# Kernel tuning notes

Hardware: AMD Instinct MI355X
Metric: run time of the kernel (lower is better)

## Reference

```python
import jax, jax.numpy as jnp
import numpy as np

N_NODES = 100000
N_EDGES = 1600000
HID = 128


def setup_inputs() -> dict:
    key = jax.random.key(0)
    ks = jax.random.split(key, 16)

    def w(k, fan_in, fan_out, scale=None):
        s = scale if scale is not None else 1.0 / np.sqrt(fan_in)
        return (jax.random.normal(k, (fan_in, fan_out), jnp.float32) * s)

    inp = {
        "h": jax.random.normal(ks[0], (N_NODES, HID), jnp.float32),
        "edge_index": jax.random.randint(ks[1], (2, N_EDGES), 0, N_NODES, jnp.int64),
        "x": jax.random.normal(ks[2], (N_NODES, 3), jnp.float32),
        "v": jax.random.normal(ks[3], (N_NODES, 3), jnp.float32),
        # edge_mlp: Linear(257,128) -> ReLU -> Linear(128,128) -> ReLU
        "we1": w(ks[4], 2 * HID + 1, HID), "be1": jnp.zeros((HID,), jnp.float32),
        "we2": w(ks[5], HID, HID), "be2": jnp.zeros((HID,), jnp.float32),
        # node_mlp: Linear(384,128) -> ReLU -> Linear(128,128)
        "wn1": w(ks[6], 3 * HID, HID), "bn1": jnp.zeros((HID,), jnp.float32),
        "wn2": w(ks[7], HID, HID), "bn2": jnp.zeros((HID,), jnp.float32),
        # coord_mlp_vel: Linear(128,128) -> ReLU -> Linear(128,1)
        "wv1": w(ks[8], HID, HID), "bv1": jnp.zeros((HID,), jnp.float32),
        "wv2": w(ks[9], HID, 1), "bv2": jnp.zeros((1,), jnp.float32),
        # coord_mlp: Linear(128,128) -> ReLU -> Linear(128,1, bias=False, xavier gain 0.001)
        "wc1": w(ks[10], HID, HID), "bc1": jnp.zeros((HID,), jnp.float32),
        "wc2": w(ks[11], HID, 1, scale=0.001),
    }
    return inp


def reference(h, edge_index, x, v, we1, be1, we2, be2, wn1, bn1, wn2, bn2,
              wv1, bv1, wv2, bv2, wc1, bc1, wc2):
    n = h.shape[0]
    row, col = edge_index[0], edge_index[1]

    # coord2radial
    coord_diff = x[row] - x[col]                                  # [M, 3]
    radial = jnp.sum(coord_diff * coord_diff, axis=1, keepdims=True)  # [M, 1]

    # edge_model (no attention, no edge_attr)
    e_in = jnp.concatenate([h[row], h[col], radial], axis=1)      # [M, 257]
    edge_feat = jax.nn.relu(jax.nn.relu(e_in @ we1 + be1) @ we2 + be2)  # [M, 128]

    # coord_model: per-edge scalar gate, clamp, segment-mean over row
    gate = jax.nn.relu(edge_feat @ wc1 + bc1) @ wc2               # [M, 1]
    trans = jnp.clip(coord_diff * gate, -100.0, 100.0)            # [M, 3]
    num = jax.ops.segment_sum(trans, row, num_segments=n)         # [N, 3]
    cnt = jax.ops.segment_sum(jnp.ones_like(trans), row, num_segments=n)
    f = (num / jnp.maximum(cnt, 1.0)) * 1.0                       # coords_weight = 1.0

    # update: v' = gate(h) * v + f ; x' = x + v'
    vel_gate = jax.nn.relu(h @ wv1 + bv1) @ wv2 + bv2             # [N, 1]
    v_new = vel_gate * v + f
    x_new = x + v_new

    # node_model with others=h: cat[h, h, segment_sum(edge_feat)]
    agg = jax.ops.segment_sum(edge_feat, row, num_segments=n)     # [N, 128]
    n_in = jnp.concatenate([h, h, agg], axis=1)                   # [N, 384]
    h_new = h + (jax.nn.relu(n_in @ wn1 + bn1) @ wn2 + bn2)       # recurrent residual

    return h_new, x_new, v_new
```

## Files before the change

kernel.cpp:

```cpp
#include <hip/hip_runtime.h>
#include <hip/hip_bf16.h>
#include <stdint.h>

typedef __bf16 bf16_t;
typedef __bf16 bf16x8 __attribute__((ext_vector_type(8)));
typedef float f32x4 __attribute__((ext_vector_type(4)));

#define HID 128

__device__ __forceinline__ bf16_t* swz(bf16_t* base, int row, int rowBytes, int byteInRow) {
    return (bf16_t*)((char*)base + row * rowBytes + (byteInRow ^ ((row & 7) << 4)));
}
__device__ __forceinline__ const bf16_t* swzc(const bf16_t* base, int row, int rowBytes, int byteInRow) {
    return (const bf16_t*)((const char*)base + row * rowBytes + (byteInRow ^ ((row & 7) << 4)));
}

__device__ __forceinline__ bf16x8 pack8(float4 a, float4 b) {
    bf16x8 r;
    r[0] = (bf16_t)a.x; r[1] = (bf16_t)a.y; r[2] = (bf16_t)a.z; r[3] = (bf16_t)a.w;
    r[4] = (bf16_t)b.x; r[5] = (bf16_t)b.y; r[6] = (bf16_t)b.z; r[7] = (bf16_t)b.w;
    return r;
}

__device__ __forceinline__ bool is_i64(const int* ei) {
    return ((ei[1] | ei[3] | ei[5] | ei[7]) == 0);
}
__device__ __forceinline__ int eidx(const int* __restrict__ ei, int i, bool i64) {
    return i64 ? ei[2 * i] : ei[i];
}

__global__ void prep_kernel(const float* __restrict__ we1, const float* __restrict__ we2,
                            const float* __restrict__ wc1, const float* __restrict__ wn1,
                            const float* __restrict__ wn2, const float* __restrict__ wv1,
                            bf16_t* w1t, float* w1last, bf16_t* w2t, bf16_t* wc1t,
                            bf16_t* wn1t, bf16_t* wn2t, bf16_t* wv1t) {
    int idx = blockIdx.x * 256 + threadIdx.x;
    if (idx < 32768) { int j = idx >> 8, k = idx & 255; w1t[idx] = (bf16_t)we1[k * 128 + j]; return; }
    idx -= 32768;
    if (idx < 128) { w1last[idx] = we1[256 * 128 + idx]; return; }
    idx -= 128;
    if (idx < 16384) { int j = idx >> 7, k = idx & 127; w2t[idx] = (bf16_t)we2[k * 128 + j]; return; }
    idx -= 16384;
    if (idx < 16384) { int j = idx >> 7, k = idx & 127; wc1t[idx] = (bf16_t)wc1[k * 128 + j]; return; }
    idx -= 16384;
    if (idx < 32768) {
        int j = idx >> 8, k = idx & 255;
        float val = (k < 128) ? (wn1[k * 128 + j] + wn1[(k + 128) * 128 + j])
                              : wn1[(k + 128) * 128 + j];
        wn1t[idx] = (bf16_t)val; return;
    }
    idx -= 32768;
    if (idx < 16384) { int j = idx >> 7, k = idx & 127; wn2t[idx] = (bf16_t)wn2[k * 128 + j]; return; }
    idx -= 16384;
    if (idx < 16384) { int j = idx >> 7, k = idx & 127; wv1t[idx] = (bf16_t)wv1[k * 128 + j]; return; }
}

__global__ void hist_kernel(const int* __restrict__ ei, int* __restrict__ hist, int M) {
    const bool i64 = is_i64(ei);
    int e = blockIdx.x * 256 + threadIdx.x;
    if (e < M) atomicAdd(&hist[eidx(ei, e, i64)], 1);
}

#define NCHUNK 128
__global__ void scanA_kernel(const int* __restrict__ hist, int* __restrict__ chunk_sums,
                             int N, int CHUNK) {
    __shared__ int red[256];
    int b = blockIdx.x, tid = threadIdx.x;
    int lo = b * CHUNK, hi = min(N, lo + CHUNK);
    int s = 0;
    for (int i = lo + tid; i < hi; i += 256) s += hist[i];
    red[tid] = s; __syncthreads();
    for (int ofs = 128; ofs > 0; ofs >>= 1) {
        if (tid < ofs) red[tid] += red[tid + ofs];
        __syncthreads();
    }
    if (tid == 0) chunk_sums[b] = red[0];
}

__global__ void scanB_kernel(const int* __restrict__ chunk_sums, int* __restrict__ chunk_base,
                             int* __restrict__ off, int N, int M) {
    __shared__ int s[NCHUNK];
    int tid = threadIdx.x;
    if (tid < NCHUNK) s[tid] = chunk_sums[tid];
    __syncthreads();
    if (tid == 0) {
        int run = 0;
        for (int i = 0; i < NCHUNK; i++) { int v = s[i]; s[i] = run; run += v; }
        off[N] = M;
    }
    __syncthreads();
    if (tid < NCHUNK) chunk_base[tid] = s[tid];
}

__global__ void scanC_kernel(const int* __restrict__ hist, const int* __restrict__ chunk_base,
                             int* __restrict__ off, int* __restrict__ cursor, int N, int CHUNK) {
    __shared__ int sd[256];
    int b = blockIdx.x, tid = threadIdx.x;
    int carry = chunk_base[b];
    for (int base = 0; base < CHUNK; base += 256) {
        int li = base + tid;
        int i = b * CHUNK + li;
        int v = (li < CHUNK && i < N) ? hist[i] : 0;
        sd[tid] = v; __syncthreads();
        for (int ofs = 1; ofs < 256; ofs <<= 1) {
            int t = (tid >= ofs) ? sd[tid - ofs] : 0;
            __syncthreads();
            sd[tid] += t;
            __syncthreads();
        }
        int excl = sd[tid] - v;
        if (li < CHUNK && i < N) { off[i] = carry + excl; cursor[i] = carry + excl; }
        carry += sd[255];
        __syncthreads();
    }
}

__global__ void scatter_kernel(const int* __restrict__ ei, int* __restrict__ cursor,
                               int* __restrict__ sorted_eid, int* __restrict__ sorted_row, int M) {
    const bool i64 = is_i64(ei);
    int e = blockIdx.x * 256 + threadIdx.x;
    if (e < M) {
        int r = eidx(ei, e, i64);
        int p = atomicAdd(&cursor[r], 1);
        sorted_eid[p] = e;
        sorted_row[p] = r;
    }
}

__global__ __launch_bounds__(512, 2) void edge_kernel(
    const float* __restrict__ h, const int* __restrict__ ei, const float* __restrict__ x,
    const float* __restrict__ be1, const float* __restrict__ be2,
    const float* __restrict__ bc1, const float* __restrict__ wc2,
    const bf16_t* __restrict__ w1t, const float* __restrict__ w1last,
    const bf16_t* __restrict__ w2t, const bf16_t* __restrict__ wc1t,
    const int* __restrict__ sorted_eid, const int* __restrict__ sorted_row,
    float* __restrict__ agg, float* __restrict__ num,
    int M, int N) {
    __shared__ bf16_t lw1[128 * 256];
    __shared__ bf16_t lw2[128 * 128];
    __shared__ bf16_t lbuf[8][2][16 * 128];

    const int tid = threadIdx.x;
    for (int c = tid; c < 4096; c += 512) {
        int row = c >> 5, cin = c & 31;
        *(float4*)swz(lw1, row, 512, cin * 16) = ((const float4*)w1t)[c];
    }
    for (int c = tid; c < 2048; c += 512) {
        int row = c >> 4, cin = c & 15;
        *(float4*)swz(lw2, row, 256, cin * 16) = ((const float4*)w2t)[c];
    }
    __syncthreads();

    const bool i64 = is_i64(ei);
    const int wave = tid >> 6, lane = tid & 63;
    const int l15 = lane & 15, l4 = lane >> 4;
    bf16_t* b0 = lbuf[wave][0];
    bf16_t* b1 = lbuf[wave][1];
    const int wid = blockIdx.x * 8 + wave;
    const int nw = gridDim.x * 8;
    const int ntiles = M >> 4;
    const int K = (ntiles + nw - 1) / nw;
    const int tb = wid * K;
    const int te = min(ntiles, tb + K);

    const int c0 = lane, c1 = lane + 64;
    int carryRow = -1;
    float cs0 = 0.f, cs1 = 0.f;

    for (int t = tb; t < te; t++) {
        const int e0 = t << 4;
        const int s = lane >> 2, p = lane & 3;
        const int er = sorted_row[e0 + s];
        const int eid = sorted_eid[e0 + s];
        const int ec = eidx(ei, M + eid, i64);
        const float* hr = h + (size_t)er * HID + p * 32;
        const float* hc = h + (size_t)ec * HID + p * 32;
#pragma unroll
        for (int c2 = 0; c2 < 4; c2++) {
            float4 a = *(const float4*)(hr + c2 * 8);
            float4 b = *(const float4*)(hr + c2 * 8 + 4);
            *(bf16x8*)swz(b0, s, 256, (p * 4 + c2) * 16) = pack8(a, b);
        }
#pragma unroll
        for (int c2 = 0; c2 < 4; c2++) {
            float4 a = *(const float4*)(hc + c2 * 8);
            float4 b = *(const float4*)(hc + c2 * 8 + 4);
            *(bf16x8*)swz(b1, s, 256, (p * 4 + c2) * 16) = pack8(a, b);
        }
        float d0 = x[er * 3 + 0] - x[ec * 3 + 0];
        float d1 = x[er * 3 + 1] - x[ec * 3 + 1];
        float d2 = x[er * 3 + 2] - x[ec * 3 + 2];
        float radial = d0 * d0 + d1 * d1 + d2 * d2;
        __builtin_amdgcn_wave_barrier();

        float rad4[4];
#pragma unroll
        for (int r = 0; r < 4; r++) rad4[r] = __shfl(radial, (l4 * 4 + r) * 4, 64);

        f32x4 acc[8];
#pragma unroll
        for (int n = 0; n < 8; n++) {
            int j = n * 16 + l15;
            float bb = be1[j], wl = w1last[j];
#pragma unroll
            for (int r = 0; r < 4; r++) acc[n][r] = bb + rad4[r] * wl;
        }
#pragma unroll
        for (int kk = 0; kk < 8; kk++) {
            const bf16_t* ab = (kk < 4) ? b0 : b1;
            bf16x8 af = *(const bf16x8*)swzc(ab, l15, 256, (kk & 3) * 64 + l4 * 16);
#pragma unroll
            for (int n = 0; n < 8; n++) {
                bf16x8 bf = *(const bf16x8*)swzc(lw1, n * 16 + l15, 512, kk * 64 + l4 * 16);
                acc[n] = __builtin_amdgcn_mfma_f32_16x16x32_bf16(af, bf, acc[n], 0, 0, 0);
            }
        }
#pragma unroll
        for (int n = 0; n < 8; n++) {
#pragma unroll
            for (int r = 0; r < 4; r++) {
                int rw = l4 * 4 + r;
                *swz(b0, rw, 256, (n * 16 + l15) * 2) = (bf16_t)fmaxf(acc[n][r], 0.f);
            }
        }
        __builtin_amdgcn_wave_barrier();

        f32x4 acc2[8];
#pragma unroll
        for (int n = 0; n < 8; n++) {
            float bb = be2[n * 16 + l15];
#pragma unroll
            for (int r = 0; r < 4; r++) acc2[n][r] = bb;
        }
#pragma unroll
        for (int kk = 0; kk < 4; kk++) {
            bf16x8 af = *(const bf16x8*)swzc(b0, l15, 256, kk * 64 + l4 * 16);
#pragma unroll
            for (int n = 0; n < 8; n++) {
                bf16x8 bf = *(const bf16x8*)swzc(lw2, n * 16 + l15, 256, kk * 64 + l4 * 16);
                acc2[n] = __builtin_amdgcn_mfma_f32_16x16x32_bf16(af, bf, acc2[n], 0, 0, 0);
            }
        }
#pragma unroll
        for (int n = 0; n < 8; n++) {
#pragma unroll
            for (int r = 0; r < 4; r++) {
                float v_ = fmaxf(acc2[n][r], 0.f);
                int rw = l4 * 4 + r;
                *swz(b1, rw, 256, (n * 16 + l15) * 2) = (bf16_t)v_;
            }
        }
        __builtin_amdgcn_wave_barrier();

        f32x4 acc3[8];
#pragma unroll
        for (int n = 0; n < 8; n++) {
            float bb = bc1[n * 16 + l15];
#pragma unroll
            for (int r = 0; r < 4; r++) acc3[n][r] = bb;
        }
#pragma unroll
        for (int kk = 0; kk < 4; kk++) {
            bf16x8 af = *(const bf16x8*)swzc(b1, l15, 256, kk * 64 + l4 * 16);
#pragma unroll
            for (int n = 0; n < 8; n++) {
                bf16x8 bf = *(const bf16x8*)(wc1t + (n * 16 + l15) * 128 + kk * 32 + l4 * 8);
                acc3[n] = __builtin_amdgcn_mfma_f32_16x16x32_bf16(af, bf, acc3[n], 0, 0, 0);
            }
        }
        float pr[4] = {0.f, 0.f, 0.f, 0.f};
#pragma unroll
        for (int n = 0; n < 8; n++) {
            float w = wc2[n * 16 + l15];
#pragma unroll
            for (int r = 0; r < 4; r++) pr[r] += fmaxf(acc3[n][r], 0.f) * w;
        }
#pragma unroll
        for (int m = 1; m < 16; m <<= 1) {
#pragma unroll
            for (int r = 0; r < 4; r++) pr[r] += __shfl_xor(pr[r], m, 16);
        }

        {
            int s3 = s & 3;
            float g = (s3 == 0) ? pr[0] : ((s3 == 1) ? pr[1] : ((s3 == 2) ? pr[2] : pr[3]));
            if ((lane & 3) == 0) {
                float t0 = fminf(fmaxf(d0 * g, -100.f), 100.f);
                float t1 = fminf(fmaxf(d1 * g, -100.f), 100.f);
                float t2 = fminf(fmaxf(d2 * g, -100.f), 100.f);
                atomicAdd(num + (size_t)er * 3 + 0, t0);
                atomicAdd(num + (size_t)er * 3 + 1, t1);
                atomicAdd(num + (size_t)er * 3 + 2, t2);
            }
        }

        int er16[16];
#pragma unroll
        for (int rw = 0; rw < 16; rw++) er16[rw] = __shfl(er, rw * 4, 64);

#pragma unroll
        for (int rw = 0; rw < 16; rw++) {
            int r = er16[rw];
            if (r != carryRow) {
                if (carryRow >= 0) {
                    atomicAdd(agg + (size_t)carryRow * HID + c0, cs0);
                    atomicAdd(agg + (size_t)carryRow * HID + c1, cs1);
                }
                carryRow = r; cs0 = 0.f; cs1 = 0.f;
            }
            cs0 += (float)*swzc(b1, rw, 256, c0 * 2);
            cs1 += (float)*swzc(b1, rw, 256, c1 * 2);
        }
        __builtin_amdgcn_wave_barrier();
    }
    if (carryRow >= 0) {
        atomicAdd(agg + (size_t)carryRow * HID + c0, cs0);
        atomicAdd(agg + (size_t)carryRow * HID + c1, cs1);
    }
}

__global__ __launch_bounds__(1024, 4) void node_kernel(
    const float* __restrict__ h, const float* __restrict__ x, const float* __restrict__ v,
    const float* __restrict__ bn1, const float* __restrict__ bn2,
    const float* __restrict__ bv1, const float* __restrict__ bv2,
    const float* __restrict__ wv2,
    const bf16_t* __restrict__ wn1t, const bf16_t* __restrict__ wn2t,
    const bf16_t* __restrict__ wv1t,
    const float* __restrict__ num, const int* __restrict__ off,
    float* __restrict__ out_h, float* __restrict__ out_x, float* __restrict__ out_v,
    int N) {
    __shared__ bf16_t lw1[128 * 256];
    __shared__ bf16_t lw2[128 * 128];
    __shared__ bf16_t lbuf[16][16 * 128];

    const int tid = threadIdx.x;
    for (int c = tid; c < 4096; c += 1024) {
        int row = c >> 5, cin = c & 31;
        *(float4*)swz(lw1, row, 512, cin * 16) = ((const float4*)wn1t)[c];
    }
    for (int c = tid; c < 2048; c += 1024) {
        int row = c >> 4, cin = c & 15;
        *(float4*)swz(lw2, row, 256, cin * 16) = ((const float4*)wn2t)[c];
    }
    __syncthreads();

    const int wave = tid >> 6, lane = tid & 63;
    const int l15 = lane & 15, l4 = lane >> 4;
    bf16_t* b0 = lbuf[wave];
    const int wid = blockIdx.x * 16 + wave;
    const int stride = gridDim.x * 16;
    const int nt = N >> 4;

    for (int t = wid; t < nt; t += stride) {
        const int m0 = t << 4;
        const float* hb = h + (size_t)(m0 + l15) * HID;
        const float* ab = out_h + (size_t)(m0 + l15) * HID;

        f32x4 av[8];
#pragma unroll
        for (int n = 0; n < 8; n++) {
            float bb = bv1[n * 16 + l15];
#pragma unroll
            for (int r = 0; r < 4; r++) av[n][r] = bb;
        }
#pragma unroll
        for (int kk = 0; kk < 4; kk++) {
            const float* ap = hb + kk * 32 + l4 * 8;
            bf16x8 af = pack8(*(const float4*)ap, *(const float4*)(ap + 4));
#pragma unroll
            for (int n = 0; n < 8; n++) {
                bf16x8 bf = *(const bf16x8*)(wv1t + (n * 16 + l15) * 128 + kk * 32 + l4 * 8);
                av[n] = __builtin_amdgcn_mfma_f32_16x16x32_bf16(af, bf, av[n], 0, 0, 0);
            }
        }
        float pv[4] = {0.f, 0.f, 0.f, 0.f};
#pragma unroll
        for (int n = 0; n < 8; n++) {
            float w = wv2[n * 16 + l15];
#pragma unroll
            for (int r = 0; r < 4; r++) pv[r] += fmaxf(av[n][r], 0.f) * w;
        }
#pragma unroll
        for (int m = 1; m < 16; m <<= 1) {
#pragma unroll
            for (int r = 0; r < 4; r++) pv[r] += __shfl_xor(pv[r], m, 16);
        }
        float bv2v = bv2[0];
        if (l15 == 0) {
#pragma unroll
            for (int r = 0; r < 4; r++) {
                int m = m0 + l4 * 4 + r;
                float vg = pv[r] + bv2v;
                float c = (float)(off[m + 1] - off[m]);
                float inv = 1.0f / fmaxf(c, 1.0f);
#pragma unroll
                for (int i = 0; i < 3; i++) {
                    float f = num[(size_t)m * 3 + i] * inv;
                    float vn = vg * v[(size_t)m * 3 + i] + f;
                    out_v[(size_t)m * 3 + i] = vn;
                    out_x[(size_t)m * 3 + i] = x[(size_t)m * 3 + i] + vn;
                }
            }
        }

        f32x4 a1[8];
#pragma unroll
        for (int n = 0; n < 8; n++) {
            float bb = bn1[n * 16 + l15];
#pragma unroll
            for (int r = 0; r < 4; r++) a1[n][r] = bb;
        }
#pragma unroll
        for (int kk = 0; kk < 4; kk++) {
            const float* ap = hb + kk * 32 + l4 * 8;
            bf16x8 af = pack8(*(const float4*)ap, *(const float4*)(ap + 4));
#pragma unroll
            for (int n = 0; n < 8; n++) {
                bf16x8 bf = *(const bf16x8*)swzc(lw1, n * 16 + l15, 512, kk * 64 + l4 * 16);
                a1[n] = __builtin_amdgcn_mfma_f32_16x16x32_bf16(af, bf, a1[n], 0, 0, 0);
            }
        }
#pragma unroll
        for (int c2 = 0; c2 < 4; c2++) {
            const float* ap = ab + c2 * 32 + l4 * 8;
            float fa[8];
            *(float4*)fa = *(const float4*)ap;
            *(float4*)(fa + 4) = *(const float4*)(ap + 4);
            bf16x8 hi8, lo8;
#pragma unroll
            for (int i = 0; i < 8; i++) {
                bf16_t hi = (bf16_t)fa[i];
                hi8[i] = hi;
                lo8[i] = (bf16_t)(fa[i] - (float)hi);
            }
#pragma unroll
            for (int n = 0; n < 8; n++) {
                bf16x8 bfh = *(const bf16x8*)swzc(lw1, n * 16 + l15, 512, (4 + c2) * 64 + l4 * 16);
                a1[n] = __builtin_amdgcn_mfma_f32_16x16x32_bf16(hi8, bfh, a1[n], 0, 0, 0);
            }
#pragma unroll
            for (int n = 0; n < 8; n++) {
                bf16x8 bfl = *(const bf16x8*)swzc(lw1, n * 16 + l15, 512, (4 + c2) * 64 + l4 * 16);
                a1[n] = __builtin_amdgcn_mfma_f32_16x16x32_bf16(lo8, bfl, a1[n], 0, 0, 0);
            }
        }
#pragma unroll
        for (int n = 0; n < 8; n++) {
#pragma unroll
            for (int r = 0; r < 4; r++) {
                int rw = l4 * 4 + r;
                *swz(b0, rw, 256, (n * 16 + l15) * 2) = (bf16_t)fmaxf(a1[n][r], 0.f);
            }
        }
        __builtin_amdgcn_wave_barrier();

        f32x4 a2[8];
#pragma unroll
        for (int n = 0; n < 8; n++) {
            float bb = bn2[n * 16 + l15];
#pragma unroll
            for (int r = 0; r < 4; r++) a2[n][r] = bb;
        }
#pragma unroll
        for (int kk = 0; kk < 4; kk++) {
            bf16x8 af = *(const bf16x8*)swzc(b0, l15, 256, kk * 64 + l4 * 16);
#pragma unroll
            for (int n = 0; n < 8; n++) {
                bf16x8 bf = *(const bf16x8*)swzc(lw2, n * 16 + l15, 256, kk * 64 + l4 * 16);
                a2[n] = __builtin_amdgcn_mfma_f32_16x16x32_bf16(af, bf, a2[n], 0, 0, 0);
            }
        }
#pragma unroll
        for (int n = 0; n < 8; n++) {
            int j = n * 16 + l15;
#pragma unroll
            for (int r = 0; r < 4; r++) {
                int m = m0 + l4 * 4 + r;
                out_h[(size_t)m * HID + j] = h[(size_t)m * HID + j] + a2[n][r];
            }
        }
        __builtin_amdgcn_wave_barrier();
    }
}

extern "C" void kernel_launch(void* const* d_in, const int* in_sizes, int n_in,
                              void* d_out, int out_size, void* d_ws, size_t ws_size,
                              hipStream_t stream) {
    const float* h   = (const float*)d_in[0];
    const int*   ei  = (const int*)d_in[1];
    const float* x   = (const float*)d_in[2];
    const float* v   = (const float*)d_in[3];
    const float* we1 = (const float*)d_in[4];
    const float* be1 = (const float*)d_in[5];
    const float* we2 = (const float*)d_in[6];
    const float* be2 = (const float*)d_in[7];
    const float* wn1 = (const float*)d_in[8];
    const float* bn1 = (const float*)d_in[9];
    const float* wn2 = (const float*)d_in[10];
    const float* bn2 = (const float*)d_in[11];
    const float* wv1 = (const float*)d_in[12];
    const float* bv1 = (const float*)d_in[13];
    const float* wv2 = (const float*)d_in[14];
    const float* bv2 = (const float*)d_in[15];
    const float* wc1 = (const float*)d_in[16];
    const float* bc1 = (const float*)d_in[17];
    const float* wc2 = (const float*)d_in[18];

    const int N = in_sizes[0] / HID;
    const int M = in_sizes[1] / 2;

    float* out_h = (float*)d_out;
    float* out_x = out_h + (size_t)N * HID;
    float* out_v = out_x + (size_t)N * 3;

    char* ws = (char*)d_ws;
    auto align256 = [](size_t v) { return (v + 255) & ~(size_t)255; };
    size_t o = 0;
    bf16_t* w1t    = (bf16_t*)(ws + o); o += 65536;
    float*  w1last = (float*)(ws + o);  o += 512;
    bf16_t* w2t    = (bf16_t*)(ws + o); o += 32768;
    bf16_t* wc1t   = (bf16_t*)(ws + o); o += 32768;
    bf16_t* wn1t   = (bf16_t*)(ws + o); o += 65536;
    bf16_t* wn2t   = (bf16_t*)(ws + o); o += 32768;
    bf16_t* wv1t   = (bf16_t*)(ws + o); o += 32768;
    float*  num    = (float*)(ws + o);        o = align256(o + (size_t)N * 12);
    int*    hist   = (int*)(ws + o);          o = align256(o + (size_t)N * 4);
    int*    off    = (int*)(ws + o);          o = align256(o + (size_t)(N + 1) * 4);
    int*    cursor = (int*)(ws + o);          o = align256(o + (size_t)N * 4);
    int*    chunk_sums = (int*)(ws + o);      o = align256(o + NCHUNK * 4);
    int*    chunk_base = (int*)(ws + o);      o = align256(o + NCHUNK * 4);
    int*    sorted_eid = (int*)(ws + o);      o = align256(o + (size_t)M * 4);
    int*    sorted_row = (int*)(ws + o);      o = align256(o + (size_t)M * 4);

    const int CHUNK = (N + NCHUNK - 1) / NCHUNK;

    hipMemsetAsync(out_h, 0, (size_t)N * HID * sizeof(float), stream);
    hipMemsetAsync(num, 0, (size_t)N * 12, stream);
    hipMemsetAsync(hist, 0, (size_t)N * 4, stream);

    prep_kernel<<<513, 256, 0, stream>>>(we1, we2, wc1, wn1, wn2, wv1,
                                         w1t, w1last, w2t, wc1t, wn1t, wn2t, wv1t);
    hist_kernel<<<(M + 255) / 256, 256, 0, stream>>>(ei, hist, M);
    scanA_kernel<<<NCHUNK, 256, 0, stream>>>(hist, chunk_sums, N, CHUNK);
    scanB_kernel<<<1, 256, 0, stream>>>(chunk_sums, chunk_base, off, N, M);
    scanC_kernel<<<NCHUNK, 256, 0, stream>>>(hist, chunk_base, off, cursor, N, CHUNK);
    scatter_kernel<<<(M + 255) / 256, 256, 0, stream>>>(ei, cursor, sorted_eid, sorted_row, M);

    edge_kernel<<<256, 512, 0, stream>>>(h, ei, x, be1, be2, bc1, wc2,
                                         w1t, w1last, w2t, wc1t,
                                         sorted_eid, sorted_row,
                                         out_h, num, M, N);
    node_kernel<<<256, 1024, 0, stream>>>(h, x, v, bn1, bn2, bv1, bv2, wv2,
                                          wn1t, wn2t, wv1t, num, off,
                                          out_h, out_x, out_v, N);
}
```

Measured before the change: 1.597 ms.

## Halve per-wave LDS staging and raise edge kernel to 12 waves per block

The edge kernel now keeps one 16x128 bf16 LDS buffer per wave instead of two. The h[row] operand for the first GEMM is loaded straight from global memory into MFMA A-fragments rather than staged through LDS. The LDS this frees lets each block run 12 waves (768 threads), aimed at more latency hiding for the gathers and atomics. In exchange, the row features are read per fragment from global memory (sorted rows are often repeated and cached), registers are tighter under launch_bounds(768,3), and extra wave barriers are added for buffer reuse.

```diff
diff --git a/kernel.cpp b/kernel.cpp
--- a/kernel.cpp
+++ b/kernel.cpp
@@ -127,7 +127,7 @@
     }
 }
 
-__global__ __launch_bounds__(512, 2) void edge_kernel(
+__global__ __launch_bounds__(768, 3) void edge_kernel(
     const float* __restrict__ h, const int* __restrict__ ei, const float* __restrict__ x,
     const float* __restrict__ be1, const float* __restrict__ be2,
     const float* __restrict__ bc1, const float* __restrict__ wc2,
@@ -138,14 +138,14 @@
     int M, int N) {
     __shared__ bf16_t lw1[128 * 256];
     __shared__ bf16_t lw2[128 * 128];
-    __shared__ bf16_t lbuf[8][2][16 * 128];
+    __shared__ bf16_t lbuf[12][16 * 128];
 
     const int tid = threadIdx.x;
-    for (int c = tid; c < 4096; c += 512) {
+    for (int c = tid; c < 4096; c += 768) {
         int row = c >> 5, cin = c & 31;
         *(float4*)swz(lw1, row, 512, cin * 16) = ((const float4*)w1t)[c];
     }
-    for (int c = tid; c < 2048; c += 512) {
+    for (int c = tid; c < 2048; c += 768) {
         int row = c >> 4, cin = c & 15;
         *(float4*)swz(lw2, row, 256, cin * 16) = ((const float4*)w2t)[c];
     }
@@ -154,10 +154,9 @@
     const bool i64 = is_i64(ei);
     const int wave = tid >> 6, lane = tid & 63;
     const int l15 = lane & 15, l4 = lane >> 4;
-    bf16_t* b0 = lbuf[wave][0];
-    bf16_t* b1 = lbuf[wave][1];
-    const int wid = blockIdx.x * 8 + wave;
-    const int nw = gridDim.x * 8;
+    bf16_t* b0 = lbuf[wave];
+    const int wid = blockIdx.x * 12 + wave;
+    const int nw = gridDim.x * 12;
     const int ntiles = M >> 4;
     const int K = (ntiles + nw - 1) / nw;
     const int tb = wid * K;
@@ -169,27 +168,21 @@
 
     for (int t = tb; t < te; t++) {
         const int e0 = t << 4;
+        const int erl = sorted_row[e0 + l15];
         const int s = lane >> 2, p = lane & 3;
-        const int er = sorted_row[e0 + s];
-        const int eid = sorted_eid[e0 + s];
-        const int ec = eidx(ei, M + eid, i64);
-        const float* hr = h + (size_t)er * HID + p * 32;
-        const float* hc = h + (size_t)ec * HID + p * 32;
+        const int ers = sorted_row[e0 + s];
+        const int ecs = eidx(ei, M + sorted_eid[e0 + s], i64);
+
+        const float* hcs = h + (size_t)ecs * HID + p * 32;
 #pragma unroll
         for (int c2 = 0; c2 < 4; c2++) {
-            float4 a = *(const float4*)(hr + c2 * 8);
-            float4 b = *(const float4*)(hr + c2 * 8 + 4);
+            float4 a = *(const float4*)(hcs + c2 * 8);
+            float4 b = *(const float4*)(hcs + c2 * 8 + 4);
             *(bf16x8*)swz(b0, s, 256, (p * 4 + c2) * 16) = pack8(a, b);
         }
-#pragma unroll
-        for (int c2 = 0; c2 < 4; c2++) {
-            float4 a = *(const float4*)(hc + c2 * 8);
-            float4 b = *(const float4*)(hc + c2 * 8 + 4);
-            *(bf16x8*)swz(b1, s, 256, (p * 4 + c2) * 16) = pack8(a, b);
-        }
-        float d0 = x[er * 3 + 0] - x[ec * 3 + 0];
-        float d1 = x[er * 3 + 1] - x[ec * 3 + 1];
-        float d2 = x[er * 3 + 2] - x[ec * 3 + 2];
+        float d0 = x[ers * 3 + 0] - x[ecs * 3 + 0];
+        float d1 = x[ers * 3 + 1] - x[ecs * 3 + 1];
+        float d2 = x[ers * 3 + 2] - x[ecs * 3 + 2];
         float radial = d0 * d0 + d1 * d1 + d2 * d2;
         __builtin_amdgcn_wave_barrier();
 
@@ -205,16 +198,23 @@
 #pragma unroll
             for (int r = 0; r < 4; r++) acc[n][r] = bb + rad4[r] * wl;
         }
+        const float* hbr = h + (size_t)erl * HID;
 #pragma unroll
         for (int kk = 0; kk < 8; kk++) {
-            const bf16_t* ab = (kk < 4) ? b0 : b1;
-            bf16x8 af = *(const bf16x8*)swzc(ab, l15, 256, (kk & 3) * 64 + l4 * 16);
+            bf16x8 af;
+            if (kk < 4) {
+                const float* ap = hbr + kk * 32 + l4 * 8;
+                af = pack8(*(const float4*)ap, *(const float4*)(ap + 4));
+            } else {
+                af = *(const bf16x8*)swzc(b0, l15, 256, (kk & 3) * 64 + l4 * 16);
+            }
 #pragma unroll
             for (int n = 0; n < 8; n++) {
                 bf16x8 bf = *(const bf16x8*)swzc(lw1, n * 16 + l15, 512, kk * 64 + l4 * 16);
                 acc[n] = __builtin_amdgcn_mfma_f32_16x16x32_bf16(af, bf, acc[n], 0, 0, 0);
             }
         }
+        __builtin_amdgcn_wave_barrier();
 #pragma unroll
         for (int n = 0; n < 8; n++) {
 #pragma unroll
@@ -241,13 +241,14 @@
                 acc2[n] = __builtin_amdgcn_mfma_f32_16x16x32_bf16(af, bf, acc2[n], 0, 0, 0);
             }
         }
+        __builtin_amdgcn_wave_barrier();
 #pragma unroll
         for (int n = 0; n < 8; n++) {
 #pragma unroll
             for (int r = 0; r < 4; r++) {
                 float v_ = fmaxf(acc2[n][r], 0.f);
                 int rw = l4 * 4 + r;
-                *swz(b1, rw, 256, (n * 16 + l15) * 2) = (bf16_t)v_;
+                *swz(b0, rw, 256, (n * 16 + l15) * 2) = (bf16_t)v_;
             }
         }
         __builtin_amdgcn_wave_barrier();
@@ -261,7 +262,7 @@
         }
 #pragma unroll
         for (int kk = 0; kk < 4; kk++) {
-            bf16x8 af = *(const bf16x8*)swzc(b1, l15, 256, kk * 64 + l4 * 16);
+            bf16x8 af = *(const bf16x8*)swzc(b0, l15, 256, kk * 64 + l4 * 16);
 #pragma unroll
             for (int n = 0; n < 8; n++) {
                 bf16x8 bf = *(const bf16x8*)(wc1t + (n * 16 + l15) * 128 + kk * 32 + l4 * 8);
@@ -288,15 +289,15 @@
                 float t0 = fminf(fmaxf(d0 * g, -100.f), 100.f);
                 float t1 = fminf(fmaxf(d1 * g, -100.f), 100.f);
                 float t2 = fminf(fmaxf(d2 * g, -100.f), 100.f);
-                atomicAdd(num + (size_t)er * 3 + 0, t0);
-                atomicAdd(num + (size_t)er * 3 + 1, t1);
-                atomicAdd(num + (size_t)er * 3 + 2, t2);
+                atomicAdd(num + (size_t)ers * 3 + 0, t0);
+                atomicAdd(num + (size_t)ers * 3 + 1, t1);
+                atomicAdd(num + (size_t)ers * 3 + 2, t2);
             }
         }
 
         int er16[16];
 #pragma unroll
-        for (int rw = 0; rw < 16; rw++) er16[rw] = __shfl(er, rw * 4, 64);
+        for (int rw = 0; rw < 16; rw++) er16[rw] = __shfl(erl, rw, 64);
 
 #pragma unroll
         for (int rw = 0; rw < 16; rw++) {
@@ -308,8 +309,8 @@
                 }
                 carryRow = r; cs0 = 0.f; cs1 = 0.f;
             }
-            cs0 += (float)*swzc(b1, rw, 256, c0 * 2);
-            cs1 += (float)*swzc(b1, rw, 256, c1 * 2);
+            cs0 += (float)*swzc(b0, rw, 256, c0 * 2);
+            cs1 += (float)*swzc(b0, rw, 256, c1 * 2);
         }
         __builtin_amdgcn_wave_barrier();
     }
@@ -546,7 +547,7 @@
     scanC_kernel<<<NCHUNK, 256, 0, stream>>>(hist, chunk_base, off, cursor, N, CHUNK);
     scatter_kernel<<<(M + 255) / 256, 256, 0, stream>>>(ei, cursor, sorted_eid, sorted_row, M);
 
-    edge_kernel<<<256, 512, 0, stream>>>(h, ei, x, be1, be2, bc1, wc2,
+    edge_kernel<<<256, 768, 0, stream>>>(h, ei, x, be1, be2, bc1, wc2,
                                          w1t, w1last, w2t, wc1t,
                                          sorted_eid, sorted_row,
                                          out_h, num, M, N);
```

Measured after the change: 1.799 ms. 1.13x slower.

## Partition edges at row boundaries to replace atomics with plain stores

Applied to the files above, without the earlier changes.

Each wave now gets an edge range aligned to segment boundaries, found by binary search over the row offsets, so no destination row is shared between waves. That makes the per-row agg and num accumulations exclusive, and the atomicAdds become plain stores. The coordinate-gate sum is also carried in registers per row instead of being issued as three atomics per edge. The cost is partial tiles at range ends (clamped loads, masked rows), a little load imbalance, and the binary-search setup.

```diff
diff --git a/kernel.cpp b/kernel.cpp
--- a/kernel.cpp
+++ b/kernel.cpp
@@ -134,6 +134,7 @@
     const bf16_t* __restrict__ w1t, const float* __restrict__ w1last,
     const bf16_t* __restrict__ w2t, const bf16_t* __restrict__ wc1t,
     const int* __restrict__ sorted_eid, const int* __restrict__ sorted_row,
+    const int* __restrict__ off,
     float* __restrict__ agg, float* __restrict__ num,
     int M, int N) {
     __shared__ bf16_t lw1[128 * 256];
@@ -158,20 +159,28 @@
     bf16_t* b1 = lbuf[wave][1];
     const int wid = blockIdx.x * 8 + wave;
     const int nw = gridDim.x * 8;
-    const int ntiles = M >> 4;
-    const int K = (ntiles + nw - 1) / nw;
-    const int tb = wid * K;
-    const int te = min(ntiles, tb + K);
+
+    long long tgt_b = ((long long)wid * M) / nw;
+    long long tgt_e = ((long long)(wid + 1) * M) / nw;
+    int lo = 0, hi = N;
+    while (lo < hi) { int mid = (lo + hi) >> 1; if (off[mid] >= (int)tgt_b) hi = mid; else lo = mid + 1; }
+    const int eb = off[lo];
+    lo = 0; hi = N;
+    while (lo < hi) { int mid = (lo + hi) >> 1; if (off[mid] >= (int)tgt_e) hi = mid; else lo = mid + 1; }
+    const int ee = off[lo];
 
     const int c0 = lane, c1 = lane + 64;
     int carryRow = -1;
     float cs0 = 0.f, cs1 = 0.f;
-
-    for (int t = tb; t < te; t++) {
-        const int e0 = t << 4;
+    float n0 = 0.f, n1 = 0.f, n2 = 0.f;
+
+    const int ntl = (ee - eb + 15) >> 4;
+    for (int t = 0; t < ntl; t++) {
+        const int e0 = eb + (t << 4);
         const int s = lane >> 2, p = lane & 3;
-        const int er = sorted_row[e0 + s];
-        const int eid = sorted_eid[e0 + s];
+        const int es = min(e0 + s, ee - 1);
+        const int er = sorted_row[es];
+        const int eid = sorted_eid[es];
         const int ec = eidx(ei, M + eid, i64);
         const float* hr = h + (size_t)er * HID + p * 32;
         const float* hc = h + (size_t)ec * HID + p * 32;
@@ -281,17 +290,13 @@
             for (int r = 0; r < 4; r++) pr[r] += __shfl_xor(pr[r], m, 16);
         }
 
+        float t0, t1, t2;
         {
             int s3 = s & 3;
             float g = (s3 == 0) ? pr[0] : ((s3 == 1) ? pr[1] : ((s3 == 2) ? pr[2] : pr[3]));
-            if ((lane & 3) == 0) {
-                float t0 = fminf(fmaxf(d0 * g, -100.f), 100.f);
-                float t1 = fminf(fmaxf(d1 * g, -100.f), 100.f);
-                float t2 = fminf(fmaxf(d2 * g, -100.f), 100.f);
-                atomicAdd(num + (size_t)er * 3 + 0, t0);
-                atomicAdd(num + (size_t)er * 3 + 1, t1);
-                atomicAdd(num + (size_t)er * 3 + 2, t2);
-            }
+            t0 = fminf(fmaxf(d0 * g, -100.f), 100.f);
+            t1 = fminf(fmaxf(d1 * g, -100.f), 100.f);
+            t2 = fminf(fmaxf(d2 * g, -100.f), 100.f);
         }
 
         int er16[16];
@@ -300,22 +305,39 @@
 
 #pragma unroll
         for (int rw = 0; rw < 16; rw++) {
-            int r = er16[rw];
-            if (r != carryRow) {
-                if (carryRow >= 0) {
-                    atomicAdd(agg + (size_t)carryRow * HID + c0, cs0);
-                    atomicAdd(agg + (size_t)carryRow * HID + c1, cs1);
+            if (e0 + rw < ee) {
+                int r = er16[rw];
+                float u0 = __shfl(t0, rw * 4, 64);
+                float u1 = __shfl(t1, rw * 4, 64);
+                float u2 = __shfl(t2, rw * 4, 64);
+                if (r != carryRow) {
+                    if (carryRow >= 0) {
+                        agg[(size_t)carryRow * HID + c0] = cs0;
+                        agg[(size_t)carryRow * HID + c1] = cs1;
+                        if (lane == 0) {
+                            num[(size_t)carryRow * 3 + 0] = n0;
+                            num[(size_t)carryRow * 3 + 1] = n1;
+                            num[(size_t)carryRow * 3 + 2] = n2;
+                        }
+                    }
+                    carryRow = r;
+                    cs0 = 0.f; cs1 = 0.f; n0 = 0.f; n1 = 0.f; n2 = 0.f;
                 }
-                carryRow = r; cs0 = 0.f; cs1 = 0.f;
-            }
-            cs0 += (float)*swzc(b1, rw, 256, c0 * 2);
-            cs1 += (float)*swzc(b1, rw, 256, c1 * 2);
+                cs0 += (float)*swzc(b1, rw, 256, c0 * 2);
+                cs1 += (float)*swzc(b1, rw, 256, c1 * 2);
+                n0 += u0; n1 += u1; n2 += u2;
+            }
         }
         __builtin_amdgcn_wave_barrier();
     }
     if (carryRow >= 0) {
-        atomicAdd(agg + (size_t)carryRow * HID + c0, cs0);
-        atomicAdd(agg + (size_t)carryRow * HID + c1, cs1);
+        agg[(size_t)carryRow * HID + c0] = cs0;
+        agg[(size_t)carryRow * HID + c1] = cs1;
+        if (lane == 0) {
+            num[(size_t)carryRow * 3 + 0] = n0;
+            num[(size_t)carryRow * 3 + 1] = n1;
+            num[(size_t)carryRow * 3 + 2] = n2;
+        }
     }
 }
 
@@ -548,7 +570,7 @@
 
     edge_kernel<<<256, 512, 0, stream>>>(h, ei, x, be1, be2, bc1, wc2,
                                          w1t, w1last, w2t, wc1t,
-                                         sorted_eid, sorted_row,
+                                         sorted_eid, sorted_row, off,
                                          out_h, num, M, N);
     node_kernel<<<256, 1024, 0, stream>>>(h, x, v, bn1, bn2, bv1, bv2, wv2,
                                           wn1t, wn2t, wv1t, num, off,
```

Measured after the change: 1.936 ms. 21.3% more time.
